# Performance work log

Measured on AMD Instinct MI355X. Metric: run time of the kernel, lower is better.

Reference implementation:

```python
import jax, jax.numpy as jnp
import numpy as np

B, D_IMG, H, VOCAB, T = 16384, 2048, 512, 200, 20

def setup_inputs() -> dict:
    key = jax.random.key(0)
    ks = jax.random.split(key, 24)
    def w(k, shape, scale=0.05):
        return jax.random.normal(k, shape, dtype=jnp.float32) * scale
    return {
        "images": jax.random.normal(ks[0], (B, D_IMG), dtype=jnp.float32),
        "actions": jax.random.randint(ks[1], (B, T), 0, VOCAB, dtype=jnp.int64),
        # encoder: Linear(2048,512) -> ReLU -> Linear(512,512)
        "enc_w1": w(ks[2], (H, D_IMG)), "enc_b1": jnp.zeros((H,), jnp.float32),
        "enc_w2": w(ks[3], (H, H)),     "enc_b2": jnp.zeros((H,), jnp.float32),
        # GRUCell(512,512): gate order r, z, n (PyTorch convention)
        "gru_wih": w(ks[4], (3 * H, H)), "gru_bih": jnp.zeros((3 * H,), jnp.float32),
        "gru_whh": w(ks[5], (3 * H, H)), "gru_bhh": jnp.zeros((3 * H,), jnp.float32),
        # actor: 512->64->64->vocab
        "act_w1": w(ks[6], (64, H)),   "act_b1": jnp.zeros((64,), jnp.float32),
        "act_w2": w(ks[7], (64, 64)),  "act_b2": jnp.zeros((64,), jnp.float32),
        "act_w3": w(ks[8], (VOCAB, 64), 0.01), "act_b3": jnp.zeros((VOCAB,), jnp.float32),
        # critic: 512->64->64->1
        "cri_w1": w(ks[9], (64, H)),   "cri_b1": jnp.zeros((64,), jnp.float32),
        "cri_w2": w(ks[10], (64, 64)), "cri_b2": jnp.zeros((64,), jnp.float32),
        "cri_w3": w(ks[11], (1, 64), 0.02), "cri_b3": jnp.zeros((1,), jnp.float32),
    }

def reference(images, actions, enc_w1, enc_b1, enc_w2, enc_b2,
              gru_wih, gru_bih, gru_whh, gru_bhh,
              act_w1, act_b1, act_w2, act_b2, act_w3, act_b3,
              cri_w1, cri_b1, cri_w2, cri_b2, cri_w3, cri_b3):
    # encoder
    x = jax.nn.relu(images @ enc_w1.T + enc_b1) @ enc_w2.T + enc_b2  # [B, H]
    # input-side GRU gates are constant across steps (same x every step)
    xg = x @ gru_wih.T + gru_bih                                     # [B, 3H]
    xr, xz, xn = jnp.split(xg, 3, axis=-1)

    def step(hx, a_t):
        hg = hx @ gru_whh.T + gru_bhh
        hr, hz, hn = jnp.split(hg, 3, axis=-1)
        r = jax.nn.sigmoid(xr + hr)
        z = jax.nn.sigmoid(xz + hz)
        n = jnp.tanh(xn + r * hn)
        hx = (1.0 - z) * n + z * hx                                   # [B, H]
        # actor head -> categorical stats
        a_h = jnp.tanh(jnp.tanh(hx @ act_w1.T + act_b1) @ act_w2.T + act_b2)
        logits = a_h @ act_w3.T + act_b3                              # [B, V]
        logp = jax.nn.log_softmax(logits, axis=-1)
        lp = jnp.take_along_axis(logp, a_t[:, None], axis=1)[:, 0]    # [B]
        ent = -jnp.sum(jnp.exp(logp) * logp, axis=-1)                 # [B]
        # critic head
        c_h = jnp.tanh(jnp.tanh(hx @ cri_w1.T + cri_b1) @ cri_w2.T + cri_b2)
        v = c_h @ cri_w3.T + cri_b3                                   # [B, 1]
        return hx, (lp, ent, v)

    hx0 = jnp.zeros_like(x)
    _, (lps, ents, vs) = jax.lax.scan(step, hx0, actions.T)           # [T, B, ...]
    logprobs = lps.T                                                  # [B, T]
    entropies = ents.T                                                # [B, T]
    values = jnp.transpose(vs, (1, 0, 2))                             # [B, T, 1]
    return actions, logprobs, entropies, values
```

## Files before the change

kernel.cpp:

```cpp
#include <hip/hip_runtime.h>
#include <hip/hip_fp16.h>
#include <cstddef>
#include <cstdint>

#define BB 16384
#define DIMG 2048
#define HH 512
#define VOCAB 200
#define TT 20

using frag16 = __attribute__((ext_vector_type(8))) short;
using f32x4v = __attribute__((ext_vector_type(4))) float;

#define MFMA16(a, b, c) __builtin_amdgcn_mfma_f32_16x16x32_bf16((a), (b), (c), 0, 0, 0)

__device__ __forceinline__ float bf2f(unsigned short u) {
    union { unsigned int i; float f; } c; c.i = ((unsigned int)u) << 16; return c.f;
}
__device__ __forceinline__ unsigned short f2bf(float f) {
    union { float f; unsigned int i; } c; c.f = f;
    unsigned int u = c.i;
    u = (u + 0x7FFFu + ((u >> 16) & 1u)) >> 16;
    return (unsigned short)u;
}
__device__ __forceinline__ float sigf(float x) { return 1.f / (1.f + __expf(-x)); }
__device__ __forceinline__ float ftanh(float x) {
    return 1.f - 2.f / (1.f + __expf(2.f * x));
}
__device__ __forceinline__ void gload16(const void* g, void* l) {
    __builtin_amdgcn_global_load_lds(
        (__attribute__((address_space(1))) void*)g,
        (__attribute__((address_space(3))) void*)l, 16, 0, 0);
}

template<int ACT, int OM>
__global__ __launch_bounds__(256) void gemm_bt_mfma(
    const unsigned short* __restrict__ A, const unsigned short* __restrict__ W,
    const float* __restrict__ bias, void* __restrict__ Cv, int M, int N, int K)
{
    __shared__ unsigned short As[128 * 32];
    __shared__ unsigned short Ws[128 * 32];
    const int t = threadIdx.x;
    const int lane = t & 63, w = t >> 6;
    const int bm = blockIdx.x, bn = blockIdx.y;
    const int wm = (w >> 1) * 64, wn = (w & 1) * 64;

    f32x4v acc[4][4];
    #pragma unroll
    for (int i = 0; i < 4; ++i)
        #pragma unroll
        for (int j = 0; j < 4; ++j)
            #pragma unroll
            for (int r = 0; r < 4; ++r) acc[i][j][r] = 0.f;

    const unsigned short* Ag  = A + (size_t)(bm * 128 + (t >> 2)) * K + (t & 3) * 8;
    const unsigned short* Ag2 = A + (size_t)(bm * 128 + 64 + (t >> 2)) * K + (t & 3) * 8;
    const unsigned short* Wg  = W + (size_t)(bn * 128 + (t >> 2)) * K + (t & 3) * 8;
    const unsigned short* Wg2 = W + (size_t)(bn * 128 + 64 + (t >> 2)) * K + (t & 3) * 8;
    char* AsB = (char*)As; char* WsB = (char*)Ws;

    const int kIters = K >> 5;
    for (int ki = 0; ki < kIters; ++ki) {
        const int k0 = ki * 32;
        gload16(Ag  + k0, AsB + w * 1024);
        gload16(Ag2 + k0, AsB + 4096 + w * 1024);
        gload16(Wg  + k0, WsB + w * 1024);
        gload16(Wg2 + k0, WsB + 4096 + w * 1024);
        __syncthreads();
        frag16 af[4], bf[4];
        #pragma unroll
        for (int i = 0; i < 4; ++i) {
            af[i] = *(const frag16*)(AsB + (wm + i * 16 + (lane & 15)) * 64 + (lane >> 4) * 16);
            bf[i] = *(const frag16*)(WsB + (wn + i * 16 + (lane & 15)) * 64 + (lane >> 4) * 16);
        }
        #pragma unroll
        for (int i = 0; i < 4; ++i)
            #pragma unroll
            for (int j = 0; j < 4; ++j)
                acc[i][j] = MFMA16(af[i], bf[j], acc[i][j]);
        __syncthreads();
    }

    #pragma unroll
    for (int j = 0; j < 4; ++j) {
        const int gn = bn * 128 + wn + j * 16 + (lane & 15);
        const float bv = bias[gn];
        #pragma unroll
        for (int i = 0; i < 4; ++i) {
            #pragma unroll
            for (int r = 0; r < 4; ++r) {
                const size_t gm = (size_t)(bm * 128 + wm + i * 16 + (lane >> 4) * 4 + r);
                float v = acc[i][j][r] + bv;
                if (ACT == 1) v = fmaxf(v, 0.f);
                if (OM == 0)      ((float*)Cv)[gm * N + gn] = v;
                else if (OM == 1) ((unsigned short*)Cv)[gm * N + gn] = f2bf(v);
                else              ((__half*)Cv)[gm * N + gn] = __float2half(v);
            }
        }
    }
}

__device__ __forceinline__ void gru_body(
    unsigned short* lds,
    const unsigned short* __restrict__ hb, unsigned short* __restrict__ hob,
    const unsigned short* __restrict__ whhb, const float* __restrict__ bhh,
    const __half* __restrict__ xg, int bm, int bn, int t)
{
    char* L = (char*)lds;
    const int lane = t & 63, w = t >> 6;
    const int q = lane >> 4, m = lane & 15;

    f32x4v acc[3][4];
    #pragma unroll
    for (int g = 0; g < 3; ++g)
        #pragma unroll
        for (int j = 0; j < 4; ++j)
            #pragma unroll
            for (int r = 0; r < 4; ++r) acc[g][j][r] = 0.f;

    const unsigned short* Ag = hb + (size_t)(bm * 64 + (t >> 2)) * HH + (t & 3) * 8;
    const unsigned short* Wg0 = whhb + (size_t)(0 * HH + bn * 64 + (t >> 2)) * HH + (t & 3) * 8;
    const unsigned short* Wg1 = whhb + (size_t)(1 * HH + bn * 64 + (t >> 2)) * HH + (t & 3) * 8;
    const unsigned short* Wg2 = whhb + (size_t)(2 * HH + bn * 64 + (t >> 2)) * HH + (t & 3) * 8;

    for (int ki = 0; ki < 8; ++ki) {
        const int k0 = ki * 64;
        gload16(Ag + k0,       L + w * 1024);
        gload16(Ag + k0 + 32,  L + 4096 + w * 1024);
        gload16(Wg0 + k0,      L + 8192 + w * 1024);
        gload16(Wg0 + k0 + 32, L + 8192 + 12288 + w * 1024);
        gload16(Wg1 + k0,      L + 8192 + 4096 + w * 1024);
        gload16(Wg1 + k0 + 32, L + 8192 + 12288 + 4096 + w * 1024);
        gload16(Wg2 + k0,      L + 8192 + 8192 + w * 1024);
        gload16(Wg2 + k0 + 32, L + 8192 + 12288 + 8192 + w * 1024);
        __syncthreads();
        #pragma unroll
        for (int kk = 0; kk < 2; ++kk) {
            frag16 af = *(const frag16*)(L + kk * 4096 + (w * 16 + m) * 64 + q * 16);
            #pragma unroll
            for (int g = 0; g < 3; ++g)
                #pragma unroll
                for (int j = 0; j < 4; ++j) {
                    frag16 bf = *(const frag16*)(L + 8192 + kk * 12288 + g * 4096 + (j * 16 + m) * 64 + q * 16);
                    acc[g][j] = MFMA16(af, bf, acc[g][j]);
                }
        }
        __syncthreads();
    }

    {
        const __half* Xg = xg + (size_t)(bm * 64 + (t >> 3)) * (3 * HH) + bn * 64 + (t & 7) * 8;
        #pragma unroll
        for (int c = 0; c < 6; ++c) {
            const int g = c >> 1, rh = c & 1;
            gload16(Xg + (size_t)rh * 32 * (3 * HH) + g * HH, L + g * 8192 + rh * 4096 + w * 1024);
        }
        const unsigned short* Hg = hb + (size_t)(bm * 64 + (t >> 3)) * HH + bn * 64 + (t & 7) * 8;
        gload16(Hg,                       L + 24576 + w * 1024);
        gload16(Hg + (size_t)32 * HH,     L + 24576 + 4096 + w * 1024);
    }
    __syncthreads();

    float br[4], bz[4], bnn[4];
    #pragma unroll
    for (int j = 0; j < 4; ++j) {
        const int gc = bn * 64 + j * 16 + m;
        br[j] = bhh[gc]; bz[j] = bhh[HH + gc]; bnn[j] = bhh[2 * HH + gc];
    }

    unsigned short hv[4][4];
    #pragma unroll
    for (int r = 0; r < 4; ++r) {
        const int row = w * 16 + q * 4 + r;
        #pragma unroll
        for (int j = 0; j < 4; ++j) {
            const int col2 = (j * 16 + m) * 2;
            const float xr = __half2float(*(const __half*)(L + row * 128 + col2));
            const float xz = __half2float(*(const __half*)(L + 8192 + row * 128 + col2));
            const float xn = __half2float(*(const __half*)(L + 16384 + row * 128 + col2));
            const float ho = bf2f(*(const unsigned short*)(L + 24576 + row * 128 + col2));
            const float rg = sigf(xr + acc[0][j][r] + br[j]);
            const float zg = sigf(xz + acc[1][j][r] + bz[j]);
            const float ng = ftanh(xn + rg * (acc[2][j][r] + bnn[j]));
            hv[r][j] = f2bf((1.f - zg) * ng + zg * ho);
        }
    }
    __syncthreads();
    #pragma unroll
    for (int r = 0; r < 4; ++r) {
        const int row = w * 16 + q * 4 + r;
        #pragma unroll
        for (int j = 0; j < 4; ++j)
            *(unsigned short*)(L + 24576 + row * 128 + (j * 16 + m) * 2) = hv[r][j];
    }
    __syncthreads();
    {
        const int sr = t >> 2, sc = (t & 3) * 16;
        uint4 v0 = *(const uint4*)(L + 24576 + sr * 128 + sc * 2);
        uint4 v1 = *(const uint4*)(L + 24576 + sr * 128 + sc * 2 + 16);
        unsigned short* dst = hob + (size_t)(bm * 64 + sr) * HH + bn * 64 + sc;
        *(uint4*)dst = v0;
        *(uint4*)(dst + 8) = v1;
    }
}

__device__ __forceinline__ void heads_body(
    unsigned short* lds, const unsigned short* __restrict__ hxb,
    const unsigned short* __restrict__ w1c, const unsigned short* __restrict__ w2s,
    const unsigned short* __restrict__ w3s,
    const float* __restrict__ b1c, const float* __restrict__ b2c,
    const float* __restrict__ b3s,
    const float* __restrict__ cw3, const float* __restrict__ cb3,
    const int* __restrict__ actions,
    float* __restrict__ out_lp, float* __restrict__ out_ent,
    float* __restrict__ out_v, int tstep, int hblk, int t)
{
    char* sH = (char*)lds;
    char* sW = (char*)lds + 4096;
    unsigned short* u1 = lds;
    const int lane = t & 63, w = t >> 6;
    const int q = lane >> 4, m = lane & 15;
    const int row0 = hblk * 32;
    const int ri = (w & 1) * 16, ch = (w >> 1) * 64;

    f32x4v acc[4];
    #pragma unroll
    for (int j = 0; j < 4; ++j)
        #pragma unroll
        for (int r = 0; r < 4; ++r) acc[j][r] = 0.f;

    const unsigned short* Hrow = hxb + (size_t)(row0 + ((t >> 2) & 31)) * HH
                                 + (t >> 7) * 32 + (t & 3) * 8;
    const unsigned short* Wrow[4]; int WldsOff[4];
    #pragma unroll
    for (int c = 0; c < 4; ++c) {
        const int kk = c & 1, rb = (c >> 1) * 64;
        Wrow[c] = w1c + (size_t)(rb + (t >> 2)) * HH + kk * 32 + (t & 3) * 8;
        WldsOff[c] = kk * 8192 + rb * 64;
    }

    for (int ki = 0; ki < 8; ++ki) {
        const int k0 = ki * 64;
        gload16(Hrow + k0, sH + w * 1024);
        #pragma unroll
        for (int c = 0; c < 4; ++c)
            gload16(Wrow[c] + k0, sW + WldsOff[c] + w * 1024);
        __syncthreads();
        #pragma unroll
        for (int kk = 0; kk < 2; ++kk) {
            frag16 af = *(const frag16*)(sH + kk * 2048 + (ri + m) * 64 + q * 16);
            #pragma unroll
            for (int j = 0; j < 4; ++j) {
                frag16 bf = *(const frag16*)(sW + kk * 8192 + (ch + j * 16 + m) * 64 + q * 16);
                acc[j] = MFMA16(af, bf, acc[j]);
            }
        }
        __syncthreads();
    }
    #pragma unroll
    for (int j = 0; j < 4; ++j) {
        const int col = ch + j * 16 + m;
        const float bv = b1c[col];
        #pragma unroll
        for (int r = 0; r < 4; ++r)
            u1[(ri + q * 4 + r) * 136 + col] = f2bf(ftanh(acc[j][r] + bv));
    }
    __syncthreads();

    f32x4v acc2[4];
    #pragma unroll
    for (int j = 0; j < 4; ++j)
        #pragma unroll
        for (int r = 0; r < 4; ++r) acc2[j][r] = 0.f;
    #pragma unroll
    for (int kk = 0; kk < 2; ++kk) {
        frag16 af2 = *(const frag16*)(u1 + (ri + m) * 136 + ch + kk * 32 + q * 8);
        #pragma unroll
        for (int j = 0; j < 4; ++j) {
            frag16 bf2 = *(const frag16*)(w2s + (size_t)(ch + j * 16 + m) * 64 + kk * 32 + q * 8);
            acc2[j] = MFMA16(af2, bf2, acc2[j]);
        }
    }
    __syncthreads();
    #pragma unroll
    for (int j = 0; j < 4; ++j) {
        const int col = ch + j * 16 + m;
        const float bv = b2c[col];
        #pragma unroll
        for (int r = 0; r < 4; ++r)
            u1[(ri + q * 4 + r) * 136 + col] = f2bf(ftanh(acc2[j][r] + bv));
    }
    __syncthreads();

    if (w < 2) {
        f32x4v acc3[13];
        #pragma unroll
        for (int j = 0; j < 13; ++j)
            #pragma unroll
            for (int r = 0; r < 4; ++r) acc3[j][r] = 0.f;
        #pragma unroll
        for (int kk = 0; kk < 2; ++kk) {
            frag16 af3 = *(const frag16*)(u1 + (w * 16 + m) * 136 + kk * 32 + q * 8);
            #pragma unroll
            for (int j = 0; j < 13; ++j) {
                frag16 bf3 = *(const frag16*)(w3s + (size_t)(j * 16 + m) * 64 + kk * 32 + q * 8);
                acc3[j] = MFMA16(af3, bf3, acc3[j]);
            }
        }
        float bcol[13];
        #pragma unroll
        for (int j = 0; j < 13; ++j) bcol[j] = b3s[j * 16 + m];
        const bool vlast = (m < 8);
        #pragma unroll
        for (int r = 0; r < 4; ++r) {
            const int gr = row0 + w * 16 + 4 * q + r;
            const int a = actions[(size_t)gr * TT + tstep];
            float lg[13], mx = -1e30f;
            #pragma unroll
            for (int j = 0; j < 13; ++j) {
                float v = acc3[j][r] + bcol[j];
                lg[j] = (j < 12 || vlast) ? v : -1e30f;
                mx = fmaxf(mx, lg[j]);
            }
            #pragma unroll
            for (int o = 1; o < 16; o <<= 1) mx = fmaxf(mx, __shfl_xor(mx, o));
            float s1 = 0.f, s2 = 0.f, sel = 0.f;
            #pragma unroll
            for (int j = 0; j < 13; ++j) {
                float e = __expf(lg[j] - mx);
                s1 += e; s2 += e * lg[j];
                sel += (j * 16 + m == a) ? lg[j] : 0.f;
            }
            #pragma unroll
            for (int o = 1; o < 16; o <<= 1) {
                s1 += __shfl_xor(s1, o); s2 += __shfl_xor(s2, o); sel += __shfl_xor(sel, o);
            }
            const float lse = mx + __logf(s1);
            if (m == 0) {
                out_lp[(size_t)gr * TT + tstep]  = sel - lse;
                out_ent[(size_t)gr * TT + tstep] = lse - s2 / s1;
            }
        }
    } else {
        const int row = (w - 2) * 16 + m;
        const unsigned short* u2row = u1 + row * 136 + 64 + q * 16;
        float pv = 0.f;
        #pragma unroll
        for (int kk = 0; kk < 16; ++kk)
            pv += bf2f(u2row[kk]) * cw3[q * 16 + kk];
        pv += __shfl_xor(pv, 16);
        pv += __shfl_xor(pv, 32);
        if (q == 0) out_v[(size_t)(row0 + row) * TT + tstep] = pv + cb3[0];
    }
}

__global__ __launch_bounds__(256, 4) void step_fused(
    const unsigned short* __restrict__ hin, unsigned short* __restrict__ hout,
    const unsigned short* __restrict__ whhb, const float* __restrict__ bhh,
    const __half* __restrict__ xg,
    const unsigned short* __restrict__ w1c, const unsigned short* __restrict__ w2s,
    const unsigned short* __restrict__ w3s,
    const float* __restrict__ b1c, const float* __restrict__ b2c,
    const float* __restrict__ b3s,
    const float* __restrict__ cw3, const float* __restrict__ cb3,
    const int* __restrict__ actions,
    float* __restrict__ out_lp, float* __restrict__ out_ent,
    float* __restrict__ out_v, int hstep)
{
    __shared__ unsigned short lds[16384];
    const int b = blockIdx.x;
    if (b < 2048) {
        gru_body(lds, hin, hout, whhb, bhh, xg, b & 255, b >> 8, threadIdx.x);
    } else if (hstep >= 0) {
        heads_body(lds, hin, w1c, w2s, w3s, b1c, b2c, b3s, cw3, cb3,
                   actions, out_lp, out_ent, out_v, hstep, b - 2048, threadIdx.x);
    }
}

__global__ __launch_bounds__(256) void heads_tail(
    const unsigned short* __restrict__ hx,
    const unsigned short* __restrict__ w1c, const unsigned short* __restrict__ w2s,
    const unsigned short* __restrict__ w3s,
    const float* __restrict__ b1c, const float* __restrict__ b2c,
    const float* __restrict__ b3s,
    const float* __restrict__ cw3, const float* __restrict__ cb3,
    const int* __restrict__ actions,
    float* __restrict__ out_lp, float* __restrict__ out_ent,
    float* __restrict__ out_v, int tstep)
{
    __shared__ unsigned short lds[10240];
    heads_body(lds, hx, w1c, w2s, w3s, b1c, b2c, b3s, cw3, cb3,
               actions, out_lp, out_ent, out_v, tstep, blockIdx.x, threadIdx.x);
}

__global__ void prep_heads(
    const float* __restrict__ aw1, const float* __restrict__ cw1,
    const float* __restrict__ aw2, const float* __restrict__ cw2,
    const float* __restrict__ aw3,
    const float* __restrict__ ab1, const float* __restrict__ cb1,
    const float* __restrict__ ab2, const float* __restrict__ cb2,
    const float* __restrict__ ab3,
    unsigned short* __restrict__ w1c, unsigned short* __restrict__ w2s,
    unsigned short* __restrict__ w3s,
    float* __restrict__ b1c, float* __restrict__ b2c, float* __restrict__ b3s)
{
    int i = blockIdx.x * 256 + threadIdx.x;
    if (i < 65536) { int r = i >> 9, c = i & 511;
        w1c[i] = f2bf(r < 64 ? aw1[r * 512 + c] : cw1[(r - 64) * 512 + c]); return; }
    i -= 65536;
    if (i < 8192) { int r = i >> 6, c = i & 63;
        w2s[i] = f2bf(r < 64 ? aw2[r * 64 + c] : cw2[(r - 64) * 64 + c]); return; }
    i -= 8192;
    if (i < 13312) { int r = i >> 6, c = i & 63;
        w3s[i] = f2bf(r < 200 ? aw3[r * 64 + c] : 0.f); return; }
    i -= 13312;
    if (i < 128) { b1c[i] = i < 64 ? ab1[i] : cb1[i - 64]; return; }
    i -= 128;
    if (i < 128) { b2c[i] = i < 64 ? ab2[i] : cb2[i - 64]; return; }
    i -= 128;
    if (i < 208) { b3s[i] = i < 200 ? ab3[i] : 0.f; return; }
}

__global__ void f2b_kernel(const float* __restrict__ s, unsigned short* __restrict__ d, int n) {
    int i = (blockIdx.x * 256 + threadIdx.x) * 4;
    if (i < n) {
        float4 v = *(const float4*)(s + i);
        ushort4 o;
        o.x = f2bf(v.x); o.y = f2bf(v.y); o.z = f2bf(v.z); o.w = f2bf(v.w);
        *(ushort4*)(d + i) = o;
    }
}

__global__ void copy_actions(const int* __restrict__ a, float* __restrict__ o, int n) {
    int i = blockIdx.x * 256 + threadIdx.x;
    if (i < n) o[i] = (float)a[i];
}

extern "C" void kernel_launch(void* const* d_in, const int* in_sizes, int n_in,
                              void* d_out, int out_size, void* d_ws, size_t ws_size,
                              hipStream_t stream)
{
    const float* images = (const float*)d_in[0];
    const int*   actions = (const int*)d_in[1];
    const float* enc_w1 = (const float*)d_in[2];
    const float* enc_b1 = (const float*)d_in[3];
    const float* enc_w2 = (const float*)d_in[4];
    const float* enc_b2 = (const float*)d_in[5];
    const float* gru_wih = (const float*)d_in[6];
    const float* gru_bih = (const float*)d_in[7];
    const float* gru_whh = (const float*)d_in[8];
    const float* gru_bhh = (const float*)d_in[9];
    const float* act_w1 = (const float*)d_in[10];
    const float* act_b1 = (const float*)d_in[11];
    const float* act_w2 = (const float*)d_in[12];
    const float* act_b2 = (const float*)d_in[13];
    const float* act_w3 = (const float*)d_in[14];
    const float* act_b3 = (const float*)d_in[15];
    const float* cri_w1 = (const float*)d_in[16];
    const float* cri_b1 = (const float*)d_in[17];
    const float* cri_w2 = (const float*)d_in[18];
    const float* cri_b2 = (const float*)d_in[19];
    const float* cri_w3 = (const float*)d_in[20];
    const float* cri_b3 = (const float*)d_in[21];

    char* ws = (char*)d_ws;
    unsigned short* imgb = (unsigned short*)ws;
    __half*         xg   = (__half*)ws;
    unsigned short* hbA  = (unsigned short*)(ws + 67108864);
    unsigned short* hbB  = (unsigned short*)(ws + 83886080);
    unsigned short* w1b  = (unsigned short*)(ws + 100663296);
    unsigned short* w2b  = (unsigned short*)(ws + 102760448);
    unsigned short* wihb = (unsigned short*)(ws + 103284736);
    unsigned short* whhb = (unsigned short*)(ws + 104857600);
    unsigned short* w1c  = (unsigned short*)(ws + 106430464);
    unsigned short* w2s  = (unsigned short*)(ws + 106561536);
    unsigned short* w3s  = (unsigned short*)(ws + 106577920);
    float*          b1c  = (float*)(ws + 106604544);
    float*          b2c  = (float*)(ws + 106605056);
    float*          b3s  = (float*)(ws + 106605568);

    float* out_act = (float*)d_out;
    float* out_lp  = out_act + (size_t)BB * TT;
    float* out_ent = out_lp  + (size_t)BB * TT;
    float* out_v   = out_ent + (size_t)BB * TT;

    dim3 blk(256);

    f2b_kernel<<<(BB * DIMG / 4 + 255) / 256, blk, 0, stream>>>(images, imgb, BB * DIMG);
    f2b_kernel<<<(512 * DIMG / 4 + 255) / 256, blk, 0, stream>>>(enc_w1, w1b, 512 * DIMG);
    f2b_kernel<<<(512 * 512 / 4 + 255) / 256, blk, 0, stream>>>(enc_w2, w2b, 512 * 512);
    f2b_kernel<<<(3 * HH * HH / 4 + 255) / 256, blk, 0, stream>>>(gru_wih, wihb, 3 * HH * HH);
    f2b_kernel<<<(3 * HH * HH / 4 + 255) / 256, blk, 0, stream>>>(gru_whh, whhb, 3 * HH * HH);
    prep_heads<<<(87504 + 255) / 256, blk, 0, stream>>>(
        act_w1, cri_w1, act_w2, cri_w2, act_w3,
        act_b1, cri_b1, act_b2, cri_b2, act_b3,
        w1c, w2s, w3s, b1c, b2c, b3s);

    gemm_bt_mfma<1, 1><<<dim3(BB / 128, 4), blk, 0, stream>>>(imgb, w1b, enc_b1, hbA, BB, 512, DIMG);
    gemm_bt_mfma<0, 1><<<dim3(BB / 128, 4), blk, 0, stream>>>(hbA, w2b, enc_b2, hbB, BB, 512, HH);
    gemm_bt_mfma<0, 2><<<dim3(BB / 128, 12), blk, 0, stream>>>(hbB, wihb, gru_bih, xg, BB, 1536, HH);

    hipMemsetAsync(hbA, 0, (size_t)BB * HH * 2, stream);
    copy_actions<<<(BB * TT + 255) / 256, blk, 0, stream>>>(actions, out_act, BB * TT);

    for (int t = 0; t < TT; ++t) {
        const unsigned short* hin = (t & 1) ? hbB : hbA;
        unsigned short*      hout = (t & 1) ? hbA : hbB;
        step_fused<<<2560, blk, 0, stream>>>(hin, hout, whhb, gru_bhh, xg,
            w1c, w2s, w3s, b1c, b2c, b3s, cri_w3, cri_b3, actions,
            out_lp, out_ent, out_v, t - 1);
    }
    heads_tail<<<512, blk, 0, stream>>>((TT & 1) ? hbB : hbA, w1c, w2s, w3s,
        b1c, b2c, b3s, cri_w3, cri_b3, actions, out_lp, out_ent, out_v, TT - 1);
}
```

Before: 1.523 ms.

## Double GRU row tile to 128 rows so each W_hh fragment feeds two MFMAs

```diff
diff --git a/kernel.cpp b/kernel.cpp
--- a/kernel.cpp
+++ b/kernel.cpp
@@ -106,101 +106,111 @@
     const unsigned short* __restrict__ whhb, const float* __restrict__ bhh,
     const __half* __restrict__ xg, int bm, int bn, int t)
 {
-    char* L = (char*)lds;
+    char* L  = (char*)lds;
+    char* LW = L + 16384;
     const int lane = t & 63, w = t >> 6;
     const int q = lane >> 4, m = lane & 15;
 
-    f32x4v acc[3][4];
-    #pragma unroll
-    for (int g = 0; g < 3; ++g)
-        #pragma unroll
-        for (int j = 0; j < 4; ++j)
-            #pragma unroll
-            for (int r = 0; r < 4; ++r) acc[g][j][r] = 0.f;
-
-    const unsigned short* Ag = hb + (size_t)(bm * 64 + (t >> 2)) * HH + (t & 3) * 8;
+    f32x4v acc[2][3][4];
+    #pragma unroll
+    for (int i = 0; i < 2; ++i)
+        #pragma unroll
+        for (int g = 0; g < 3; ++g)
+            #pragma unroll
+            for (int j = 0; j < 4; ++j)
+                #pragma unroll
+                for (int r = 0; r < 4; ++r) acc[i][g][j][r] = 0.f;
+
+    const unsigned short* Ag  = hb + (size_t)(bm * 128 + (t >> 2)) * HH + (t & 3) * 8;
     const unsigned short* Wg0 = whhb + (size_t)(0 * HH + bn * 64 + (t >> 2)) * HH + (t & 3) * 8;
     const unsigned short* Wg1 = whhb + (size_t)(1 * HH + bn * 64 + (t >> 2)) * HH + (t & 3) * 8;
     const unsigned short* Wg2 = whhb + (size_t)(2 * HH + bn * 64 + (t >> 2)) * HH + (t & 3) * 8;
 
     for (int ki = 0; ki < 8; ++ki) {
         const int k0 = ki * 64;
-        gload16(Ag + k0,       L + w * 1024);
-        gload16(Ag + k0 + 32,  L + 4096 + w * 1024);
-        gload16(Wg0 + k0,      L + 8192 + w * 1024);
-        gload16(Wg0 + k0 + 32, L + 8192 + 12288 + w * 1024);
-        gload16(Wg1 + k0,      L + 8192 + 4096 + w * 1024);
-        gload16(Wg1 + k0 + 32, L + 8192 + 12288 + 4096 + w * 1024);
-        gload16(Wg2 + k0,      L + 8192 + 8192 + w * 1024);
-        gload16(Wg2 + k0 + 32, L + 8192 + 12288 + 8192 + w * 1024);
+        gload16(Ag + k0,                          L + w * 1024);
+        gload16(Ag + k0 + 32,                     L + 8192 + w * 1024);
+        gload16(Ag + (size_t)64 * HH + k0,        L + 4096 + w * 1024);
+        gload16(Ag + (size_t)64 * HH + k0 + 32,   L + 8192 + 4096 + w * 1024);
+        gload16(Wg0 + k0,      LW + w * 1024);
+        gload16(Wg0 + k0 + 32, LW + 12288 + w * 1024);
+        gload16(Wg1 + k0,      LW + 4096 + w * 1024);
+        gload16(Wg1 + k0 + 32, LW + 12288 + 4096 + w * 1024);
+        gload16(Wg2 + k0,      LW + 8192 + w * 1024);
+        gload16(Wg2 + k0 + 32, LW + 12288 + 8192 + w * 1024);
         __syncthreads();
         #pragma unroll
         for (int kk = 0; kk < 2; ++kk) {
-            frag16 af = *(const frag16*)(L + kk * 4096 + (w * 16 + m) * 64 + q * 16);
+            frag16 af0 = *(const frag16*)(L + kk * 8192 +        (w * 16 + m) * 64 + q * 16);
+            frag16 af1 = *(const frag16*)(L + kk * 8192 + 4096 + (w * 16 + m) * 64 + q * 16);
             #pragma unroll
             for (int g = 0; g < 3; ++g)
                 #pragma unroll
                 for (int j = 0; j < 4; ++j) {
-                    frag16 bf = *(const frag16*)(L + 8192 + kk * 12288 + g * 4096 + (j * 16 + m) * 64 + q * 16);
-                    acc[g][j] = MFMA16(af, bf, acc[g][j]);
+                    frag16 bf = *(const frag16*)(LW + kk * 12288 + g * 4096 + (j * 16 + m) * 64 + q * 16);
+                    acc[0][g][j] = MFMA16(af0, bf, acc[0][g][j]);
+                    acc[1][g][j] = MFMA16(af1, bf, acc[1][g][j]);
                 }
         }
         __syncthreads();
     }
 
-    {
-        const __half* Xg = xg + (size_t)(bm * 64 + (t >> 3)) * (3 * HH) + bn * 64 + (t & 7) * 8;
+    float br[4], bz[4], bnn[4];
+    #pragma unroll
+    for (int j = 0; j < 4; ++j) {
+        const int gc = bn * 64 + j * 16 + m;
+        br[j] = bhh[gc]; bz[j] = bhh[HH + gc]; bnn[j] = bhh[2 * HH + gc];
+    }
+
+    #pragma unroll
+    for (int half = 0; half < 2; ++half) {
+        const int rbase = bm * 128 + half * 64;
+        const __half* Xg = xg + (size_t)(rbase + (t >> 3)) * (3 * HH) + bn * 64 + (t & 7) * 8;
         #pragma unroll
         for (int c = 0; c < 6; ++c) {
             const int g = c >> 1, rh = c & 1;
             gload16(Xg + (size_t)rh * 32 * (3 * HH) + g * HH, L + g * 8192 + rh * 4096 + w * 1024);
         }
-        const unsigned short* Hg = hb + (size_t)(bm * 64 + (t >> 3)) * HH + bn * 64 + (t & 7) * 8;
-        gload16(Hg,                       L + 24576 + w * 1024);
-        gload16(Hg + (size_t)32 * HH,     L + 24576 + 4096 + w * 1024);
-    }
-    __syncthreads();
-
-    float br[4], bz[4], bnn[4];
-    #pragma unroll
-    for (int j = 0; j < 4; ++j) {
-        const int gc = bn * 64 + j * 16 + m;
-        br[j] = bhh[gc]; bz[j] = bhh[HH + gc]; bnn[j] = bhh[2 * HH + gc];
-    }
-
-    unsigned short hv[4][4];
-    #pragma unroll
-    for (int r = 0; r < 4; ++r) {
-        const int row = w * 16 + q * 4 + r;
-        #pragma unroll
-        for (int j = 0; j < 4; ++j) {
-            const int col2 = (j * 16 + m) * 2;
-            const float xr = __half2float(*(const __half*)(L + row * 128 + col2));
-            const float xz = __half2float(*(const __half*)(L + 8192 + row * 128 + col2));
-            const float xn = __half2float(*(const __half*)(L + 16384 + row * 128 + col2));
-            const float ho = bf2f(*(const unsigned short*)(L + 24576 + row * 128 + col2));
-            const float rg = sigf(xr + acc[0][j][r] + br[j]);
-            const float zg = sigf(xz + acc[1][j][r] + bz[j]);
-            const float ng = ftanh(xn + rg * (acc[2][j][r] + bnn[j]));
-            hv[r][j] = f2bf((1.f - zg) * ng + zg * ho);
-        }
-    }
-    __syncthreads();
-    #pragma unroll
-    for (int r = 0; r < 4; ++r) {
-        const int row = w * 16 + q * 4 + r;
-        #pragma unroll
-        for (int j = 0; j < 4; ++j)
-            *(unsigned short*)(L + 24576 + row * 128 + (j * 16 + m) * 2) = hv[r][j];
-    }
-    __syncthreads();
-    {
-        const int sr = t >> 2, sc = (t & 3) * 16;
-        uint4 v0 = *(const uint4*)(L + 24576 + sr * 128 + sc * 2);
-        uint4 v1 = *(const uint4*)(L + 24576 + sr * 128 + sc * 2 + 16);
-        unsigned short* dst = hob + (size_t)(bm * 64 + sr) * HH + bn * 64 + sc;
-        *(uint4*)dst = v0;
-        *(uint4*)(dst + 8) = v1;
+        const unsigned short* Hg = hb + (size_t)(rbase + (t >> 3)) * HH + bn * 64 + (t & 7) * 8;
+        gload16(Hg,                   L + 24576 + w * 1024);
+        gload16(Hg + (size_t)32 * HH, L + 24576 + 4096 + w * 1024);
+        __syncthreads();
+
+        unsigned short hv[4][4];
+        #pragma unroll
+        for (int r = 0; r < 4; ++r) {
+            const int row = w * 16 + q * 4 + r;
+            #pragma unroll
+            for (int j = 0; j < 4; ++j) {
+                const int col2 = (j * 16 + m) * 2;
+                const float xr = __half2float(*(const __half*)(L + row * 128 + col2));
+                const float xz = __half2float(*(const __half*)(L + 8192 + row * 128 + col2));
+                const float xn = __half2float(*(const __half*)(L + 16384 + row * 128 + col2));
+                const float ho = bf2f(*(const unsigned short*)(L + 24576 + row * 128 + col2));
+                const float rg = sigf(xr + acc[half][0][j][r] + br[j]);
+                const float zg = sigf(xz + acc[half][1][j][r] + bz[j]);
+                const float ng = ftanh(xn + rg * (acc[half][2][j][r] + bnn[j]));
+                hv[r][j] = f2bf((1.f - zg) * ng + zg * ho);
+            }
+        }
+        __syncthreads();
+        #pragma unroll
+        for (int r = 0; r < 4; ++r) {
+            const int row = w * 16 + q * 4 + r;
+            #pragma unroll
+            for (int j = 0; j < 4; ++j)
+                *(unsigned short*)(L + 24576 + row * 128 + (j * 16 + m) * 2) = hv[r][j];
+        }
+        __syncthreads();
+        {
+            const int sr = t >> 2, sc = (t & 3) * 16;
+            uint4 v0 = *(const uint4*)(L + 24576 + sr * 128 + sc * 2);
+            uint4 v1 = *(const uint4*)(L + 24576 + sr * 128 + sc * 2 + 16);
+            unsigned short* dst = hob + (size_t)(rbase + sr) * HH + bn * 64 + sc;
+            *(uint4*)dst = v0;
+            *(uint4*)(dst + 8) = v1;
+        }
+        __syncthreads();
     }
 }
 
@@ -354,7 +364,7 @@
     }
 }
 
-__global__ __launch_bounds__(256, 4) void step_fused(
+__global__ __launch_bounds__(256, 3) void step_fused(
     const unsigned short* __restrict__ hin, unsigned short* __restrict__ hout,
     const unsigned short* __restrict__ whhb, const float* __restrict__ bhh,
     const __half* __restrict__ xg,
@@ -367,13 +377,13 @@
     float* __restrict__ out_lp, float* __restrict__ out_ent,
     float* __restrict__ out_v, int hstep)
 {
-    __shared__ unsigned short lds[16384];
+    __shared__ unsigned short lds[20480];
     const int b = blockIdx.x;
-    if (b < 2048) {
-        gru_body(lds, hin, hout, whhb, bhh, xg, b & 255, b >> 8, threadIdx.x);
+    if (b < 1024) {
+        gru_body(lds, hin, hout, whhb, bhh, xg, b & 127, b >> 7, threadIdx.x);
     } else if (hstep >= 0) {
         heads_body(lds, hin, w1c, w2s, w3s, b1c, b2c, b3s, cw3, cb3,
-                   actions, out_lp, out_ent, out_v, hstep, b - 2048, threadIdx.x);
+                   actions, out_lp, out_ent, out_v, hstep, b - 1024, threadIdx.x);
     }
 }
 
@@ -506,7 +516,7 @@
     for (int t = 0; t < TT; ++t) {
         const unsigned short* hin = (t & 1) ? hbB : hbA;
         unsigned short*      hout = (t & 1) ? hbA : hbB;
-        step_fused<<<2560, blk, 0, stream>>>(hin, hout, whhb, gru_bhh, xg,
+        step_fused<<<1536, blk, 0, stream>>>(hin, hout, whhb, gru_bhh, xg,
             w1c, w2s, w3s, b1c, b2c, b3s, cri_w3, cri_b3, actions,
             out_lp, out_ent, out_v, t - 1);
     }
```

Result: faster. 1.429 ms (-6.2%).

## Keep GRU weight slice resident in LDS and stream hidden rows through registers

Applied to the files above, without the earlier changes.

```diff
diff --git a/kernel.cpp b/kernel.cpp
--- a/kernel.cpp
+++ b/kernel.cpp
@@ -32,6 +32,7 @@
         (__attribute__((address_space(1))) void*)g,
         (__attribute__((address_space(3))) void*)l, 16, 0, 0);
 }
+
 
 template<int ACT, int OM>
 __global__ __launch_bounds__(256) void gemm_bt_mfma(
@@ -104,103 +105,80 @@
     unsigned short* lds,
     const unsigned short* __restrict__ hb, unsigned short* __restrict__ hob,
     const unsigned short* __restrict__ whhb, const float* __restrict__ bhh,
-    const __half* __restrict__ xg, int bm, int bn, int t)
+    const __half* __restrict__ xg, int grp, int bn, int t)
 {
     char* L = (char*)lds;
     const int lane = t & 63, w = t >> 6;
     const int q = lane >> 4, m = lane & 15;
-
-    f32x4v acc[3][4];
-    #pragma unroll
-    for (int g = 0; g < 3; ++g)
-        #pragma unroll
-        for (int j = 0; j < 4; ++j)
-            #pragma unroll
-            for (int r = 0; r < 4; ++r) acc[g][j][r] = 0.f;
-
-    const unsigned short* Ag = hb + (size_t)(bm * 64 + (t >> 2)) * HH + (t & 3) * 8;
-    const unsigned short* Wg0 = whhb + (size_t)(0 * HH + bn * 64 + (t >> 2)) * HH + (t & 3) * 8;
-    const unsigned short* Wg1 = whhb + (size_t)(1 * HH + bn * 64 + (t >> 2)) * HH + (t & 3) * 8;
-    const unsigned short* Wg2 = whhb + (size_t)(2 * HH + bn * 64 + (t >> 2)) * HH + (t & 3) * 8;
-
-    for (int ki = 0; ki < 8; ++ki) {
-        const int k0 = ki * 64;
-        gload16(Ag + k0,       L + w * 1024);
-        gload16(Ag + k0 + 32,  L + 4096 + w * 1024);
-        gload16(Wg0 + k0,      L + 8192 + w * 1024);
-        gload16(Wg0 + k0 + 32, L + 8192 + 12288 + w * 1024);
-        gload16(Wg1 + k0,      L + 8192 + 4096 + w * 1024);
-        gload16(Wg1 + k0 + 32, L + 8192 + 12288 + 4096 + w * 1024);
-        gload16(Wg2 + k0,      L + 8192 + 8192 + w * 1024);
-        gload16(Wg2 + k0 + 32, L + 8192 + 12288 + 8192 + w * 1024);
-        __syncthreads();
-        #pragma unroll
-        for (int kk = 0; kk < 2; ++kk) {
-            frag16 af = *(const frag16*)(L + kk * 4096 + (w * 16 + m) * 64 + q * 16);
+    const int qs = q ^ ((m >> 1) & 3);
+    const int c0 = bn * 16;
+    const int col = c0 + m;
+
+    {
+        const int mrow = (t >> 2) & 15;
+        const int qlog = (t & 3) ^ ((t >> 3) & 3);
+        #pragma unroll
+        for (int d = 0; d < 12; ++d) {
+            const int g  = d >> 2;
+            const int kk = (d & 3) * 4 + (t >> 6);
+            gload16(whhb + (size_t)(g * HH + c0 + mrow) * HH + kk * 32 + qlog * 8,
+                    L + d * 4096 + t * 16);
+        }
+    }
+    const float br  = bhh[col];
+    const float bz  = bhh[HH + col];
+    const float bnn = bhh[2 * HH + col];
+    __syncthreads();
+
+    for (int i = 0; i < 8; ++i) {
+        const int R0 = (grp * 8 + i) * 256;
+        const unsigned short* Abase = hb + (size_t)(R0 + w * 64 + m) * HH + q * 8;
+
+        f32x4v acc[4][3];
+        #pragma unroll
+        for (int rf = 0; rf < 4; ++rf)
             #pragma unroll
             for (int g = 0; g < 3; ++g)
                 #pragma unroll
-                for (int j = 0; j < 4; ++j) {
-                    frag16 bf = *(const frag16*)(L + 8192 + kk * 12288 + g * 4096 + (j * 16 + m) * 64 + q * 16);
-                    acc[g][j] = MFMA16(af, bf, acc[g][j]);
-                }
-        }
-        __syncthreads();
-    }
-
-    {
-        const __half* Xg = xg + (size_t)(bm * 64 + (t >> 3)) * (3 * HH) + bn * 64 + (t & 7) * 8;
-        #pragma unroll
-        for (int c = 0; c < 6; ++c) {
-            const int g = c >> 1, rh = c & 1;
-            gload16(Xg + (size_t)rh * 32 * (3 * HH) + g * HH, L + g * 8192 + rh * 4096 + w * 1024);
-        }
-        const unsigned short* Hg = hb + (size_t)(bm * 64 + (t >> 3)) * HH + bn * 64 + (t & 7) * 8;
-        gload16(Hg,                       L + 24576 + w * 1024);
-        gload16(Hg + (size_t)32 * HH,     L + 24576 + 4096 + w * 1024);
-    }
-    __syncthreads();
-
-    float br[4], bz[4], bnn[4];
-    #pragma unroll
-    for (int j = 0; j < 4; ++j) {
-        const int gc = bn * 64 + j * 16 + m;
-        br[j] = bhh[gc]; bz[j] = bhh[HH + gc]; bnn[j] = bhh[2 * HH + gc];
-    }
-
-    unsigned short hv[4][4];
-    #pragma unroll
-    for (int r = 0; r < 4; ++r) {
-        const int row = w * 16 + q * 4 + r;
-        #pragma unroll
-        for (int j = 0; j < 4; ++j) {
-            const int col2 = (j * 16 + m) * 2;
-            const float xr = __half2float(*(const __half*)(L + row * 128 + col2));
-            const float xz = __half2float(*(const __half*)(L + 8192 + row * 128 + col2));
-            const float xn = __half2float(*(const __half*)(L + 16384 + row * 128 + col2));
-            const float ho = bf2f(*(const unsigned short*)(L + 24576 + row * 128 + col2));
-            const float rg = sigf(xr + acc[0][j][r] + br[j]);
-            const float zg = sigf(xz + acc[1][j][r] + bz[j]);
-            const float ng = ftanh(xn + rg * (acc[2][j][r] + bnn[j]));
-            hv[r][j] = f2bf((1.f - zg) * ng + zg * ho);
-        }
-    }
-    __syncthreads();
-    #pragma unroll
-    for (int r = 0; r < 4; ++r) {
-        const int row = w * 16 + q * 4 + r;
-        #pragma unroll
-        for (int j = 0; j < 4; ++j)
-            *(unsigned short*)(L + 24576 + row * 128 + (j * 16 + m) * 2) = hv[r][j];
-    }
-    __syncthreads();
-    {
-        const int sr = t >> 2, sc = (t & 3) * 16;
-        uint4 v0 = *(const uint4*)(L + 24576 + sr * 128 + sc * 2);
-        uint4 v1 = *(const uint4*)(L + 24576 + sr * 128 + sc * 2 + 16);
-        unsigned short* dst = hob + (size_t)(bm * 64 + sr) * HH + bn * 64 + sc;
-        *(uint4*)dst = v0;
-        *(uint4*)(dst + 8) = v1;
+                for (int r = 0; r < 4; ++r) acc[rf][g][r] = 0.f;
+
+        frag16 aA[2][4];
+        #pragma unroll
+        for (int rf = 0; rf < 4; ++rf)
+            aA[0][rf] = *(const frag16*)(Abase + (size_t)rf * 16 * HH);
+
+        #pragma unroll
+        for (int kk = 0; kk < 16; ++kk) {
+            const int cur = kk & 1, nxt = cur ^ 1;
+            if (kk < 15) {
+                #pragma unroll
+                for (int rf = 0; rf < 4; ++rf)
+                    aA[nxt][rf] = *(const frag16*)(Abase + (size_t)rf * 16 * HH + (kk + 1) * 32);
+            }
+            #pragma unroll
+            for (int g = 0; g < 3; ++g) {
+                frag16 bf = *(const frag16*)(L + g * 16384 + kk * 1024 + m * 64 + qs * 16);
+                #pragma unroll
+                for (int rf = 0; rf < 4; ++rf)
+                    acc[rf][g] = MFMA16(aA[cur][rf], bf, acc[rf][g]);
+            }
+        }
+
+        #pragma unroll
+        for (int rf = 0; rf < 4; ++rf) {
+            #pragma unroll
+            for (int r = 0; r < 4; ++r) {
+                const size_t row = (size_t)R0 + w * 64 + rf * 16 + q * 4 + r;
+                const float xr = __half2float(xg[row * (3 * HH) + col]);
+                const float xz = __half2float(xg[row * (3 * HH) + HH + col]);
+                const float xn = __half2float(xg[row * (3 * HH) + 2 * HH + col]);
+                const float ho = bf2f(hb[row * HH + col]);
+                const float rg = sigf(xr + acc[rf][0][r] + br);
+                const float zg = sigf(xz + acc[rf][1][r] + bz);
+                const float ng = ftanh(xn + rg * (acc[rf][2][r] + bnn));
+                hob[row * HH + col] = f2bf((1.f - zg) * ng + zg * ho);
+            }
+        }
     }
 }
 
@@ -220,6 +198,8 @@
     unsigned short* u1 = lds;
     const int lane = t & 63, w = t >> 6;
     const int q = lane >> 4, m = lane & 15;
+    const int qs = q ^ ((m >> 1) & 3);
+    const int scol = ((t & 3) ^ ((t >> 3) & 3)) * 8;
     const int row0 = hblk * 32;
     const int ri = (w & 1) * 16, ch = (w >> 1) * 64;
 
@@ -230,12 +210,12 @@
         for (int r = 0; r < 4; ++r) acc[j][r] = 0.f;
 
     const unsigned short* Hrow = hxb + (size_t)(row0 + ((t >> 2) & 31)) * HH
-                                 + (t >> 7) * 32 + (t & 3) * 8;
+                                 + (t >> 7) * 32 + scol;
     const unsigned short* Wrow[4]; int WldsOff[4];
     #pragma unroll
     for (int c = 0; c < 4; ++c) {
         const int kk = c & 1, rb = (c >> 1) * 64;
-        Wrow[c] = w1c + (size_t)(rb + (t >> 2)) * HH + kk * 32 + (t & 3) * 8;
+        Wrow[c] = w1c + (size_t)(rb + (t >> 2)) * HH + kk * 32 + scol;
         WldsOff[c] = kk * 8192 + rb * 64;
     }
 
@@ -248,10 +228,10 @@
         __syncthreads();
         #pragma unroll
         for (int kk = 0; kk < 2; ++kk) {
-            frag16 af = *(const frag16*)(sH + kk * 2048 + (ri + m) * 64 + q * 16);
+            frag16 af = *(const frag16*)(sH + kk * 2048 + (ri + m) * 64 + qs * 16);
             #pragma unroll
             for (int j = 0; j < 4; ++j) {
-                frag16 bf = *(const frag16*)(sW + kk * 8192 + (ch + j * 16 + m) * 64 + q * 16);
+                frag16 bf = *(const frag16*)(sW + kk * 8192 + (ch + j * 16 + m) * 64 + qs * 16);
                 acc[j] = MFMA16(af, bf, acc[j]);
             }
         }
@@ -354,7 +334,7 @@
     }
 }
 
-__global__ __launch_bounds__(256, 4) void step_fused(
+__global__ __launch_bounds__(256, 3) void step_fused(
     const unsigned short* __restrict__ hin, unsigned short* __restrict__ hout,
     const unsigned short* __restrict__ whhb, const float* __restrict__ bhh,
     const __half* __restrict__ xg,
@@ -367,13 +347,13 @@
     float* __restrict__ out_lp, float* __restrict__ out_ent,
     float* __restrict__ out_v, int hstep)
 {
-    __shared__ unsigned short lds[16384];
+    __shared__ unsigned short lds[24576];
     const int b = blockIdx.x;
-    if (b < 2048) {
-        gru_body(lds, hin, hout, whhb, bhh, xg, b & 255, b >> 8, threadIdx.x);
+    if (b < 256) {
+        gru_body(lds, hin, hout, whhb, bhh, xg, b & 7, b >> 3, threadIdx.x);
     } else if (hstep >= 0) {
         heads_body(lds, hin, w1c, w2s, w3s, b1c, b2c, b3s, cw3, cb3,
-                   actions, out_lp, out_ent, out_v, hstep, b - 2048, threadIdx.x);
+                   actions, out_lp, out_ent, out_v, hstep, b - 256, threadIdx.x);
     }
 }
 
@@ -506,7 +486,7 @@
     for (int t = 0; t < TT; ++t) {
         const unsigned short* hin = (t & 1) ? hbB : hbA;
         unsigned short*      hout = (t & 1) ? hbA : hbB;
-        step_fused<<<2560, blk, 0, stream>>>(hin, hout, whhb, gru_bhh, xg,
+        step_fused<<<768, blk, 0, stream>>>(hin, hout, whhb, gru_bhh, xg,
             w1c, w2s, w3s, b1c, b2c, b3s, cri_w3, cri_b3, actions,
             out_lp, out_ent, out_v, t - 1);
     }
```

Measured after the change: 3.796 ms. +149.2%, slower.
